# Kernel optimization log

Hardware: AMD Instinct MI355X
Metric: run time of the kernel (lower is better)

The kernel has to match this reference:

```python
import jax, jax.numpy as jnp
import numpy as np

NUM_EMBEDDINGS = 4096
EMBEDDING_DIM = 256
COMMITMENT_COST = 0.25
EPS = 1e-10


def setup_inputs() -> dict:
    key = jax.random.key(0)
    k1, k2 = jax.random.split(key)
    x = jax.random.normal(k1, (32, EMBEDDING_DIM, 32, 32), dtype=jnp.float32)
    # nn.Embedding weight init: uniform(-1/K, 1/K)
    lim = 1.0 / NUM_EMBEDDINGS
    weight = jax.random.uniform(k2, (NUM_EMBEDDINGS, EMBEDDING_DIM),
                                dtype=jnp.float32, minval=-lim, maxval=lim)
    return {"x": x, "weight": weight}


def reference(x, weight):
    B, D, H, W = x.shape
    K = weight.shape[0]
    # [B,D,H,W] -> [B,H,W,D] -> [N,D]
    flat = jnp.transpose(x, (0, 2, 3, 1)).reshape(-1, D)
    distances = (jnp.sum(flat * flat, axis=1, keepdims=True)
                 + jnp.sum(weight * weight, axis=1)
                 - 2.0 * jnp.matmul(flat, weight.T))  # [N,K]
    idx = jnp.argmin(distances, axis=1)  # [N]
    # direct gather == one_hot @ weight (same math, no NxK one-hot materialized)
    quantized = weight[idx].reshape(B, H, W, D)
    quantized = jnp.transpose(quantized, (0, 3, 1, 2))  # [B,D,H,W]
    quantized_st = x + jax.lax.stop_gradient(quantized - x)
    e_latent_loss = jnp.mean((jax.lax.stop_gradient(quantized) - x) ** 2)
    q_latent_loss = jnp.mean((quantized - jax.lax.stop_gradient(x)) ** 2)
    loss = q_latent_loss + COMMITMENT_COST * e_latent_loss
    # avg_probs = mean over tokens of one-hot encodings == normalized histogram
    counts = jnp.zeros((K,), dtype=flat.dtype).at[idx].add(1.0)
    avg_probs = counts / flat.shape[0]
    perplexity = jnp.exp(-jnp.sum(avg_probs * jnp.log(avg_probs + EPS)))
    encoding_indices = idx.reshape(B, H, W)
    return (quantized_st, loss, perplexity, encoding_indices)
```

## Files before the change

### kernel.cpp

```cpp
#include <hip/hip_runtime.h>
#include <math.h>
#include <stdint.h>

#define DIM 256
#define NUME 4096
#define NTOK 32768
#define NELEM 8388608
#define LOSS_OFF 8388608
#define PERP_OFF 8388609
#define IDX_OFF  8388610
#define MARGIN   4.0e-4f
#define ATHR_PAD 1.0e-4f
#define CAND_CAP 48
#define BOOT_TILES 32
#define TOKS 128

using short8 = __attribute__((ext_vector_type(8))) short;
using f32x16 = __attribute__((ext_vector_type(16))) float;

#define WAIT_VM4()   do { asm volatile("s_waitcnt vmcnt(4)" ::: "memory"); \
                          __builtin_amdgcn_sched_barrier(0); } while (0)
#define WAIT_VM0()   do { asm volatile("s_waitcnt vmcnt(0)" ::: "memory"); \
                          __builtin_amdgcn_sched_barrier(0); } while (0)
#define WAIT_LGKM0() do { asm volatile("s_waitcnt lgkmcnt(0)" ::: "memory"); \
                          __builtin_amdgcn_sched_barrier(0); } while (0)
#define BAR()        __builtin_amdgcn_s_barrier()

__device__ __forceinline__ uint16_t f2bf(float f) {
    uint32_t u = __float_as_uint(f);
    u += 0x7FFFu + ((u >> 16) & 1u);
    return (uint16_t)(u >> 16);
}
__device__ __forceinline__ void gload_lds16(const void* g, void* l) {
    __builtin_amdgcn_global_load_lds(
        (const __attribute__((address_space(1))) void*)g,
        (__attribute__((address_space(3))) void*)l, 16, 0, 0);
}

__global__ void vq_prep(const float* __restrict__ w, uint16_t* __restrict__ wb) {
    int gid = blockIdx.x * 256 + threadIdx.x;
    const float4* src = (const float4*)(w + (size_t)gid * 8);
    float4 a = src[0], c = src[1];
    uint4 o;
    o.x = (uint32_t)f2bf(a.x) | ((uint32_t)f2bf(a.y) << 16);
    o.y = (uint32_t)f2bf(a.z) | ((uint32_t)f2bf(a.w) << 16);
    o.z = (uint32_t)f2bf(c.x) | ((uint32_t)f2bf(c.y) << 16);
    o.w = (uint32_t)f2bf(c.z) | ((uint32_t)f2bf(c.w) << 16);
    *(uint4*)(wb + (size_t)gid * 8) = o;
}

__global__ __launch_bounds__(512, 1)
void vq_mfma(const float* __restrict__ x, const float* __restrict__ wt,
             const uint16_t* __restrict__ wb, float* __restrict__ out,
             int* __restrict__ counts, float* __restrict__ partials) {
    __shared__ __align__(16) char UB[65536];
    __shared__ float sxp[4][TOKS];
    __shared__ float sxS[TOKS];
    __shared__ unsigned gmU[TOKS];
    __shared__ unsigned candCnt[TOKS];
    __shared__ unsigned candL[TOKS * CAND_CAP];
    __shared__ int wIdxS[TOKS];
    __shared__ float lred[8];

    const int t    = threadIdx.x;
    const int lane = t & 63;
    const int wv   = t >> 6;
    const int wr   = wv >> 1, wc = wv & 1;
    const int l31  = lane & 31, hh = lane >> 5;
    const int wg   = blockIdx.x;
    const int n0   = wg << 7;
    const int b    = n0 >> 10;
    const int p0   = n0 & 1023;
    const float* xbase = x + (size_t)b * (DIM * 1024) + p0;

    if (t < TOKS) { gmU[t] = 0x7F7FFFFFu; candCnt[t] = 0; }

    {
        int tok = t & 127, w8 = t >> 7;
        const float* p = xbase + (size_t)(w8 * 64) * 1024 + tok;
        float s = 0.f;
        #pragma unroll
        for (int d = 0; d < 64; ++d) {
            float v = p[(size_t)d * 1024];
            s = fmaf(v, v, s);
            int byte = (tok << 9) + ((w8 * 64 + d) << 1);
            byte ^= ((tok & 15) << 4);
            *(uint16_t*)(UB + byte) = f2bf(v);
        }
        sxp[w8][tok] = s;
    }
    __syncthreads();
    if (t < TOKS) sxS[t] = (sxp[0][t] + sxp[1][t]) + (sxp[2][t] + sxp[3][t]);

    short8 aF[16];
    #pragma unroll
    for (int ks = 0; ks < 16; ++ks) {
        int row = wr * 32 + l31;
        int byte = (row << 9) + (ks << 5) + (hh << 4);
        byte ^= ((row & 15) << 4);
        aF[ks] = *(const short8*)(UB + byte);
    }
    __syncthreads();

    auto STAGE = [&](int k0, int half) {
        #pragma unroll
        for (int i = 0; i < 4; ++i) {
            int o16 = i * 512 + t;
            int code = o16 >> 5, u = o16 & 31;
            const char* src = (const char*)wb + ((size_t)(k0 + code) << 9)
                              + ((u ^ (code & 15)) << 4);
            gload_lds16(src, UB + (half << 15) + (o16 << 4));
        }
    };

    float run[16];
    #pragma unroll
    for (int rg = 0; rg < 16; ++rg) run[rg] = -3.0e38f;

    STAGE(0, 0);
    STAGE(64, 1);
    for (int tile = 0; tile < BOOT_TILES; ++tile) {
        if (tile < BOOT_TILES - 1) WAIT_VM4(); else WAIT_VM0();
        BAR();
        const int half = tile & 1;

        f32x16 acc = {0.f,0.f,0.f,0.f,0.f,0.f,0.f,0.f,
                      0.f,0.f,0.f,0.f,0.f,0.f,0.f,0.f};
        const int cr = wc * 32 + l31;
        const int bbase = (half << 15) + (cr << 9) + (hh << 4);
        const int bxor  = ((cr & 15) << 4);
        #pragma unroll
        for (int ks = 0; ks < 16; ++ks) {
            short8 bF = *(const short8*)(UB + ((bbase + (ks << 5)) ^ bxor));
            acc = __builtin_amdgcn_mfma_f32_32x32x16_bf16(aF[ks], bF, acc, 0, 0, 0);
        }
        #pragma unroll
        for (int rg = 0; rg < 16; ++rg) run[rg] = fmaxf(run[rg], acc[rg]);

        WAIT_LGKM0();
        BAR();
        if (tile + 2 < BOOT_TILES) STAGE((tile + 2) * 64, half);
    }

    #pragma unroll
    for (int rg = 0; rg < 16; ++rg) {
        float m = run[rg];
        #pragma unroll
        for (int sh = 1; sh < 32; sh <<= 1) m = fmaxf(m, __shfl_xor(m, sh, 64));
        if (l31 == 0) {
            int row = wr * 32 + (rg & 3) + 8 * (rg >> 2) + 4 * hh;
            float s = sxS[row] - 2.0f * m;
            atomicMin(&gmU[row], __float_as_uint(s));
        }
    }
    __syncthreads();

    float athr[16];
    #pragma unroll
    for (int rg = 0; rg < 16; ++rg) {
        int row = wr * 32 + (rg & 3) + 8 * (rg >> 2) + 4 * hh;
        athr[rg] = 0.5f * (sxS[row] - (__uint_as_float(gmU[row]) + MARGIN)) - ATHR_PAD;
    }

    STAGE(0, 0);
    STAGE(64, 1);
    for (int tile = 0; tile < 64; ++tile) {
        if (tile < 63) WAIT_VM4(); else WAIT_VM0();
        BAR();
        const int half = tile & 1;

        f32x16 acc = {0.f,0.f,0.f,0.f,0.f,0.f,0.f,0.f,
                      0.f,0.f,0.f,0.f,0.f,0.f,0.f,0.f};
        const int cr = wc * 32 + l31;
        const int bbase = (half << 15) + (cr << 9) + (hh << 4);
        const int bxor  = ((cr & 15) << 4);
        #pragma unroll
        for (int ks = 0; ks < 16; ++ks) {
            short8 bF = *(const short8*)(UB + ((bbase + (ks << 5)) ^ bxor));
            acc = __builtin_amdgcn_mfma_f32_32x32x16_bf16(aF[ks], bF, acc, 0, 0, 0);
        }
        #pragma unroll
        for (int rg = 0; rg < 16; ++rg) {
            if (acc[rg] >= athr[rg]) {
                int row = wr * 32 + (rg & 3) + 8 * (rg >> 2) + 4 * hh;
                int code = tile * 64 + wc * 32 + l31;
                unsigned s = atomicAdd(&candCnt[row], 1u);
                if (s < CAND_CAP) candL[row * CAND_CAP + s] = (unsigned)code;
            }
        }

        WAIT_LGKM0();
        BAR();
        if (tile + 2 < 64) STAGE((tile + 2) * 64, half);
    }

    float sqAcc = 0.f;
    for (int ch = 0; ch < 4; ++ch) {
        __syncthreads();
        {
            int dg = t >> 3, c = t & 7;
            #pragma unroll
            for (int it = 0; it < 4; ++it) {
                int d = it * 64 + dg;
                const float* row = xbase + (size_t)d * 1024 + ch * 32 + c * 4;
                float4 f0 = *(const float4*)(row);
                float vv[4] = {f0.x, f0.y, f0.z, f0.w};
                #pragma unroll
                for (int j = 0; j < 4; ++j) {
                    int tl = c * 4 + j;
                    *(float*)(UB + ((tl * 258 + d) << 2)) = vv[j];
                }
            }
        }
        __syncthreads();
        {
            const int grp = lane >> 4, gl = lane & 15;
            int tl = wv * 4 + grp;
            int tok = ch * 32 + tl;
            unsigned ncnt = candCnt[tok];
            int nc = (ncnt > CAND_CAP) ? 0 : (int)ncnt;
            float xr[16];
            const float* xs = (const float*)UB + tl * 258 + gl * 16;
            #pragma unroll
            for (int j = 0; j < 16; ++j) xr[j] = xs[j];
            float sxt = sxS[tok];
            float bs = 3.0e38f; int bi = 0;
            for (int ci = 0; ci < nc; ++ci) {
                int code = (int)candL[tok * CAND_CAP + ci];
                const float* wr_ = wt + (size_t)code * 256 + gl * 16;
                float p = 0.f;
                #pragma unroll
                for (int j = 0; j < 4; ++j) {
                    float4 w4 = *(const float4*)(wr_ + 4 * j);
                    p = fmaf(w4.x, xr[4 * j + 0], p);
                    p = fmaf(w4.y, xr[4 * j + 1], p);
                    p = fmaf(w4.z, xr[4 * j + 2], p);
                    p = fmaf(w4.w, xr[4 * j + 3], p);
                }
                #pragma unroll
                for (int sh = 1; sh < 16; sh <<= 1) p += __shfl_xor(p, sh, 64);
                float s = sxt - 2.0f * p;
                if (s < bs || (s == bs && code < bi)) { bs = s; bi = code; }
            }
            if (gl == 0 && nc > 0) wIdxS[tok] = bi;

            #pragma unroll
            for (int tt = 0; tt < 4; ++tt) {
                int tl2 = wv * 4 + tt;
                int tok2 = ch * 32 + tl2;
                if (candCnt[tok2] > CAND_CAP) {
                    float bs2 = 3.0e38f; int bi2 = 0;
                    for (int code = 0; code < NUME; ++code) {
                        float4 wv4 = *(const float4*)(wt + (size_t)code * 256 + lane * 4);
                        const float* xr2 = (const float*)UB + tl2 * 258 + lane * 4;
                        float p = wv4.x * xr2[0];
                        p = fmaf(wv4.y, xr2[1], p);
                        p = fmaf(wv4.z, xr2[2], p);
                        p = fmaf(wv4.w, xr2[3], p);
                        #pragma unroll
                        for (int sh = 1; sh < 64; sh <<= 1) p += __shfl_xor(p, sh, 64);
                        float s = sxS[tok2] - 2.0f * p;
                        if (s < bs2 || (s == bs2 && code < bi2)) { bs2 = s; bi2 = code; }
                    }
                    if (lane == 0) wIdxS[tok2] = bi2;
                }
            }
        }
        __syncthreads();
        {
            int tl = t & 31, db = (t >> 5) * 16;
            int idx = wIdxS[ch * 32 + tl];
            const float* wrow = wt + (size_t)idx * 256;
            float* op = out + (size_t)b * (DIM * 1024) + p0 + ch * 32 + tl;
            #pragma unroll
            for (int j = 0; j < 4; ++j) {
                int d = db + 4 * j;
                float4 q4 = *(const float4*)(wrow + d);
                const float* xr = (const float*)(UB + ((tl * 258 + d) << 2));
                float d0 = q4.x - xr[0], d1 = q4.y - xr[1];
                float d2 = q4.z - xr[2], d3 = q4.w - xr[3];
                sqAcc = fmaf(d0, d0, sqAcc); sqAcc = fmaf(d1, d1, sqAcc);
                sqAcc = fmaf(d2, d2, sqAcc); sqAcc = fmaf(d3, d3, sqAcc);
                op[(size_t)(d + 0) * 1024] = q4.x;
                op[(size_t)(d + 1) * 1024] = q4.y;
                op[(size_t)(d + 2) * 1024] = q4.z;
                op[(size_t)(d + 3) * 1024] = q4.w;
            }
        }
        if (t < 32) {
            int tok = ch * 32 + t;
            out[IDX_OFF + n0 + tok] = (float)wIdxS[tok];
            atomicAdd(&counts[wIdxS[tok]], 1);
        }
    }
    float sq = sqAcc;
    #pragma unroll
    for (int m = 32; m > 0; m >>= 1) sq += __shfl_down(sq, m, 64);
    if (lane == 0) lred[wv] = sq;
    __syncthreads();
    if (t == 0) {
        float s = ((lred[0] + lred[1]) + (lred[2] + lred[3]))
                + ((lred[4] + lred[5]) + (lred[6] + lred[7]));
        partials[wg] = s;
    }
}

#define TM 64
#define TN 64
#define DK 32
#define WS_PAD 68
__global__ __launch_bounds__(256, 2)
void vq_main_fb(const float* __restrict__ x, const float* __restrict__ wt,
                float* __restrict__ out, int* __restrict__ counts,
                float* __restrict__ partials) {
    __shared__ float As[DIM][TM];
    __shared__ float Ws[DK][WS_PAD];
    __shared__ float minv[TM];
    __shared__ int   mini[TM];
    __shared__ float sxp[4][TM];
    __shared__ float sxv[TM];
    __shared__ float lred[4];
    const int t = threadIdx.x, wg = blockIdx.x;
    const int n0 = wg * TM, b = n0 >> 10, p0 = n0 & 1023;
    const float* xb = x + (size_t)b * DIM * 1024 + p0;
    #pragma unroll
    for (int i = 0; i < 16; ++i) {
        int c = t + 256 * i, d = c >> 4, pg = (c & 15) << 2;
        *reinterpret_cast<float4*>(&As[d][pg]) =
            *reinterpret_cast<const float4*>(xb + (size_t)d * 1024 + pg);
    }
    if (t < TM) { minv[t] = 3.0e38f; mini[t] = 0; }
    __syncthreads();
    {
        int tok = t & 63, w = t >> 6;
        float p = 0.0f;
        #pragma unroll
        for (int d = 0; d < 64; ++d) { float v = As[w * 64 + d][tok]; p = fmaf(v, v, p); }
        sxp[w][tok] = p;
    }
    __syncthreads();
    if (t < TM) sxv[t] = (sxp[0][t] + sxp[1][t]) + (sxp[2][t] + sxp[3][t]);
    const int tx = t & 15, ty = t >> 4;
    for (int k0 = 0; k0 < NUME; k0 += TN) {
        float acc[4][4];
        #pragma unroll
        for (int i = 0; i < 4; ++i)
            #pragma unroll
            for (int j = 0; j < 4; ++j) acc[i][j] = 0.0f;
        for (int d0 = 0; d0 < DIM; d0 += DK) {
            __syncthreads();
            int r = t >> 3, dc = (t & 7) << 2;
            #pragma unroll
            for (int h = 0; h < 2; ++h) {
                float4 v = *reinterpret_cast<const float4*>(
                    wt + (size_t)(k0 + r + 32 * h) * DIM + d0 + dc);
                Ws[dc + 0][r + 32 * h] = v.x; Ws[dc + 1][r + 32 * h] = v.y;
                Ws[dc + 2][r + 32 * h] = v.z; Ws[dc + 3][r + 32 * h] = v.w;
            }
            __syncthreads();
            #pragma unroll
            for (int dd = 0; dd < DK; ++dd) {
                float4 a = *reinterpret_cast<const float4*>(&As[d0 + dd][ty << 2]);
                float4 w = *reinterpret_cast<const float4*>(&Ws[dd][tx << 2]);
                float av[4] = {a.x, a.y, a.z, a.w}, wv2[4] = {w.x, w.y, w.z, w.w};
                #pragma unroll
                for (int i = 0; i < 4; ++i)
                    #pragma unroll
                    for (int j = 0; j < 4; ++j) acc[i][j] = fmaf(av[i], wv2[j], acc[i][j]);
            }
        }
        #pragma unroll
        for (int i = 0; i < 4; ++i) {
            float sxt = sxv[(ty << 2) + i];
            float bv = 3.0e38f; int bi = 0;
            #pragma unroll
            for (int j = 0; j < 4; ++j) {
                float s = sxt - 2.0f * acc[i][j];
                int gi = k0 + (tx << 2) + j;
                if (s < bv) { bv = s; bi = gi; }
            }
            #pragma unroll
            for (int m = 1; m < 16; m <<= 1) {
                float ov = __shfl_xor(bv, m, 64); int oi = __shfl_xor(bi, m, 64);
                if (ov < bv || (ov == bv && oi < bi)) { bv = ov; bi = oi; }
            }
            if (tx == 0) {
                int pl = (ty << 2) + i;
                if (bv < minv[pl]) { minv[pl] = bv; mini[pl] = bi; }
            }
        }
    }
    __syncthreads();
    const int pg = (t & 15) << 2, db = t >> 4;
    int idx4[4];
    #pragma unroll
    for (int j = 0; j < 4; ++j) idx4[j] = mini[pg + j];
    float* outq = out + (size_t)b * DIM * 1024 + p0;
    float sq = 0.0f;
    #pragma unroll
    for (int i = 0; i < 16; ++i) {
        int d = db + (i << 4);
        float4 qv;
        qv.x = wt[(size_t)idx4[0] * DIM + d]; qv.y = wt[(size_t)idx4[1] * DIM + d];
        qv.z = wt[(size_t)idx4[2] * DIM + d]; qv.w = wt[(size_t)idx4[3] * DIM + d];
        float4 xa = *reinterpret_cast<const float4*>(&As[d][pg]);
        float d0_ = qv.x - xa.x, d1_ = qv.y - xa.y, d2_ = qv.z - xa.z, d3_ = qv.w - xa.w;
        sq = fmaf(d0_, d0_, sq); sq = fmaf(d1_, d1_, sq);
        sq = fmaf(d2_, d2_, sq); sq = fmaf(d3_, d3_, sq);
        *reinterpret_cast<float4*>(outq + (size_t)d * 1024 + pg) = qv;
    }
    const int lane = t & 63, wid = t >> 6;
    #pragma unroll
    for (int m = 32; m > 0; m >>= 1) sq += __shfl_down(sq, m, 64);
    if (lane == 0) lred[wid] = sq;
    __syncthreads();
    if (t == 0) partials[wg] = (lred[0] + lred[1]) + (lred[2] + lred[3]);
    if (t < TM) {
        atomicAdd(&counts[mini[t]], 1);
        out[IDX_OFF + n0 + t] = (float)mini[t];
    }
}

__global__ void vq_final(const int* __restrict__ counts,
                         const float* __restrict__ partials,
                         float* __restrict__ out, int npart) {
    __shared__ float red[256];
    int t = threadIdx.x;
    float s = 0.f;
    for (int i = t; i < npart; i += 256) s += partials[i];
    red[t] = s;
    __syncthreads();
    for (int m = 128; m > 0; m >>= 1) {
        if (t < m) red[t] += red[t + m];
        __syncthreads();
    }
    if (t == 0) out[LOSS_OFF] = 1.25f * red[0] / (float)NELEM;
    __syncthreads();
    float e = 0.0f;
    for (int c = t; c < NUME; c += 256) {
        float p = (float)counts[c] * (1.0f / (float)NTOK);
        e += p * logf(p + 1e-10f);
    }
    red[t] = e;
    __syncthreads();
    for (int m = 128; m > 0; m >>= 1) {
        if (t < m) red[t] += red[t + m];
        __syncthreads();
    }
    if (t == 0) out[PERP_OFF] = expf(-red[0]);
}

extern "C" void kernel_launch(void* const* d_in, const int* in_sizes, int n_in,
                              void* d_out, int out_size, void* d_ws, size_t ws_size,
                              hipStream_t stream) {
    const float* x  = (const float*)d_in[0];
    const float* wt = (const float*)d_in[1];
    float* out = (float*)d_out;
    const size_t WB_BYTES = (size_t)NUME * DIM * 2;
    const size_t NEED = WB_BYTES + 16384 + 2048;

    if (ws_size >= NEED) {
        uint16_t* wb  = (uint16_t*)d_ws;
        int* counts   = (int*)((char*)d_ws + WB_BYTES);
        float* partials = (float*)((char*)d_ws + WB_BYTES + 16384);
        hipMemsetAsync((char*)d_ws + WB_BYTES, 0, 16384 + 2048, stream);
        vq_prep<<<512, 256, 0, stream>>>(wt, wb);
        vq_mfma<<<NTOK / TOKS, 512, 0, stream>>>(x, wt, wb, out, counts, partials);
        vq_final<<<1, 256, 0, stream>>>(counts, partials, out, NTOK / TOKS);
    } else {
        int* counts   = (int*)d_ws;
        float* partials = (float*)((char*)d_ws + 16384);
        hipMemsetAsync(d_ws, 0, 16384 + 2048, stream);
        vq_main_fb<<<NTOK / TM, 256, 0, stream>>>(x, wt, out, counts, partials);
        vq_final<<<1, 256, 0, stream>>>(counts, partials, out, NTOK / TM);
    }
}
```

Baseline: 194.4 us.

## Halve workgroup to 4 waves, each computing two 32-row MFMA tiles per B fragment

The MFMA kernel now runs with 256 threads instead of 512, and each wave holds two A-fragment sets (64 token rows), so every B fragment read from LDS feeds two MFMAs. Staging, x-loading, rerank and output loops are widened so 4 waves cover the same work. The intent is to halve LDS B-fragment traffic per MFMA and improve MFMA issue density. In exchange it roughly doubles register pressure (accumulators, A fragments, thresholds) and halves the waves available to hide latency in the scalar rerank and epilogue phases.

```diff
diff --git a/kernel.cpp b/kernel.cpp
--- a/kernel.cpp
+++ b/kernel.cpp
@@ -18,7 +18,7 @@
 using short8 = __attribute__((ext_vector_type(8))) short;
 using f32x16 = __attribute__((ext_vector_type(16))) float;
 
-#define WAIT_VM4()   do { asm volatile("s_waitcnt vmcnt(4)" ::: "memory"); \
+#define WAIT_VM8()   do { asm volatile("s_waitcnt vmcnt(8)" ::: "memory"); \
                           __builtin_amdgcn_sched_barrier(0); } while (0)
 #define WAIT_VM0()   do { asm volatile("s_waitcnt vmcnt(0)" ::: "memory"); \
                           __builtin_amdgcn_sched_barrier(0); } while (0)
@@ -49,18 +49,18 @@
     *(uint4*)(wb + (size_t)gid * 8) = o;
 }
 
-__global__ __launch_bounds__(512, 1)
+__global__ __launch_bounds__(256, 1)
 void vq_mfma(const float* __restrict__ x, const float* __restrict__ wt,
              const uint16_t* __restrict__ wb, float* __restrict__ out,
              int* __restrict__ counts, float* __restrict__ partials) {
     __shared__ __align__(16) char UB[65536];
-    __shared__ float sxp[4][TOKS];
+    __shared__ float sxp[2][TOKS];
     __shared__ float sxS[TOKS];
     __shared__ unsigned gmU[TOKS];
     __shared__ unsigned candCnt[TOKS];
     __shared__ unsigned candL[TOKS * CAND_CAP];
     __shared__ int wIdxS[TOKS];
-    __shared__ float lred[8];
+    __shared__ float lred[4];
 
     const int t    = threadIdx.x;
     const int lane = t & 63;
@@ -77,35 +77,37 @@
 
     {
         int tok = t & 127, w8 = t >> 7;
-        const float* p = xbase + (size_t)(w8 * 64) * 1024 + tok;
+        const float* p = xbase + (size_t)(w8 * 128) * 1024 + tok;
         float s = 0.f;
         #pragma unroll
-        for (int d = 0; d < 64; ++d) {
+        for (int d = 0; d < 128; ++d) {
             float v = p[(size_t)d * 1024];
             s = fmaf(v, v, s);
-            int byte = (tok << 9) + ((w8 * 64 + d) << 1);
+            int byte = (tok << 9) + ((w8 * 128 + d) << 1);
             byte ^= ((tok & 15) << 4);
             *(uint16_t*)(UB + byte) = f2bf(v);
         }
         sxp[w8][tok] = s;
     }
     __syncthreads();
-    if (t < TOKS) sxS[t] = (sxp[0][t] + sxp[1][t]) + (sxp[2][t] + sxp[3][t]);
-
-    short8 aF[16];
-    #pragma unroll
-    for (int ks = 0; ks < 16; ++ks) {
-        int row = wr * 32 + l31;
-        int byte = (row << 9) + (ks << 5) + (hh << 4);
-        byte ^= ((row & 15) << 4);
-        aF[ks] = *(const short8*)(UB + byte);
-    }
+    if (t < TOKS) sxS[t] = sxp[0][t] + sxp[1][t];
+
+    short8 aF[2][16];
+    #pragma unroll
+    for (int rf = 0; rf < 2; ++rf)
+        #pragma unroll
+        for (int ks = 0; ks < 16; ++ks) {
+            int row = wr * 64 + rf * 32 + l31;
+            int byte = (row << 9) + (ks << 5) + (hh << 4);
+            byte ^= ((row & 15) << 4);
+            aF[rf][ks] = *(const short8*)(UB + byte);
+        }
     __syncthreads();
 
     auto STAGE = [&](int k0, int half) {
         #pragma unroll
-        for (int i = 0; i < 4; ++i) {
-            int o16 = i * 512 + t;
+        for (int i = 0; i < 8; ++i) {
+            int o16 = i * 256 + t;
             int code = o16 >> 5, u = o16 & 31;
             const char* src = (const char*)wb + ((size_t)(k0 + code) << 9)
                               + ((u ^ (code & 15)) << 4);
@@ -113,29 +115,37 @@
         }
     };
 
-    float run[16];
-    #pragma unroll
-    for (int rg = 0; rg < 16; ++rg) run[rg] = -3.0e38f;
+    float run[2][16];
+    #pragma unroll
+    for (int rf = 0; rf < 2; ++rf)
+        #pragma unroll
+        for (int rg = 0; rg < 16; ++rg) run[rf][rg] = -3.0e38f;
 
     STAGE(0, 0);
     STAGE(64, 1);
     for (int tile = 0; tile < BOOT_TILES; ++tile) {
-        if (tile < BOOT_TILES - 1) WAIT_VM4(); else WAIT_VM0();
+        if (tile < BOOT_TILES - 1) WAIT_VM8(); else WAIT_VM0();
         BAR();
         const int half = tile & 1;
 
-        f32x16 acc = {0.f,0.f,0.f,0.f,0.f,0.f,0.f,0.f,
-                      0.f,0.f,0.f,0.f,0.f,0.f,0.f,0.f};
+        f32x16 acc0 = {0.f,0.f,0.f,0.f,0.f,0.f,0.f,0.f,
+                       0.f,0.f,0.f,0.f,0.f,0.f,0.f,0.f};
+        f32x16 acc1 = {0.f,0.f,0.f,0.f,0.f,0.f,0.f,0.f,
+                       0.f,0.f,0.f,0.f,0.f,0.f,0.f,0.f};
         const int cr = wc * 32 + l31;
         const int bbase = (half << 15) + (cr << 9) + (hh << 4);
         const int bxor  = ((cr & 15) << 4);
         #pragma unroll
         for (int ks = 0; ks < 16; ++ks) {
             short8 bF = *(const short8*)(UB + ((bbase + (ks << 5)) ^ bxor));
-            acc = __builtin_amdgcn_mfma_f32_32x32x16_bf16(aF[ks], bF, acc, 0, 0, 0);
-        }
-        #pragma unroll
-        for (int rg = 0; rg < 16; ++rg) run[rg] = fmaxf(run[rg], acc[rg]);
+            acc0 = __builtin_amdgcn_mfma_f32_32x32x16_bf16(aF[0][ks], bF, acc0, 0, 0, 0);
+            acc1 = __builtin_amdgcn_mfma_f32_32x32x16_bf16(aF[1][ks], bF, acc1, 0, 0, 0);
+        }
+        #pragma unroll
+        for (int rg = 0; rg < 16; ++rg) {
+            run[0][rg] = fmaxf(run[0][rg], acc0[rg]);
+            run[1][rg] = fmaxf(run[1][rg], acc1[rg]);
+        }
 
         WAIT_LGKM0();
         BAR();
@@ -143,46 +153,59 @@
     }
 
     #pragma unroll
-    for (int rg = 0; rg < 16; ++rg) {
-        float m = run[rg];
-        #pragma unroll
-        for (int sh = 1; sh < 32; sh <<= 1) m = fmaxf(m, __shfl_xor(m, sh, 64));
-        if (l31 == 0) {
-            int row = wr * 32 + (rg & 3) + 8 * (rg >> 2) + 4 * hh;
-            float s = sxS[row] - 2.0f * m;
-            atomicMin(&gmU[row], __float_as_uint(s));
-        }
-    }
-    __syncthreads();
-
-    float athr[16];
-    #pragma unroll
-    for (int rg = 0; rg < 16; ++rg) {
-        int row = wr * 32 + (rg & 3) + 8 * (rg >> 2) + 4 * hh;
-        athr[rg] = 0.5f * (sxS[row] - (__uint_as_float(gmU[row]) + MARGIN)) - ATHR_PAD;
-    }
+    for (int rf = 0; rf < 2; ++rf)
+        #pragma unroll
+        for (int rg = 0; rg < 16; ++rg) {
+            float m = run[rf][rg];
+            #pragma unroll
+            for (int sh = 1; sh < 32; sh <<= 1) m = fmaxf(m, __shfl_xor(m, sh, 64));
+            if (l31 == 0) {
+                int row = wr * 64 + rf * 32 + (rg & 3) + 8 * (rg >> 2) + 4 * hh;
+                float s = sxS[row] - 2.0f * m;
+                atomicMin(&gmU[row], __float_as_uint(s));
+            }
+        }
+    __syncthreads();
+
+    float athr[2][16];
+    #pragma unroll
+    for (int rf = 0; rf < 2; ++rf)
+        #pragma unroll
+        for (int rg = 0; rg < 16; ++rg) {
+            int row = wr * 64 + rf * 32 + (rg & 3) + 8 * (rg >> 2) + 4 * hh;
+            athr[rf][rg] = 0.5f * (sxS[row] - (__uint_as_float(gmU[row]) + MARGIN)) - ATHR_PAD;
+        }
 
     STAGE(0, 0);
     STAGE(64, 1);
     for (int tile = 0; tile < 64; ++tile) {
-        if (tile < 63) WAIT_VM4(); else WAIT_VM0();
+        if (tile < 63) WAIT_VM8(); else WAIT_VM0();
         BAR();
         const int half = tile & 1;
 
-        f32x16 acc = {0.f,0.f,0.f,0.f,0.f,0.f,0.f,0.f,
-                      0.f,0.f,0.f,0.f,0.f,0.f,0.f,0.f};
+        f32x16 acc0 = {0.f,0.f,0.f,0.f,0.f,0.f,0.f,0.f,
+                       0.f,0.f,0.f,0.f,0.f,0.f,0.f,0.f};
+        f32x16 acc1 = {0.f,0.f,0.f,0.f,0.f,0.f,0.f,0.f,
+                       0.f,0.f,0.f,0.f,0.f,0.f,0.f,0.f};
         const int cr = wc * 32 + l31;
         const int bbase = (half << 15) + (cr << 9) + (hh << 4);
         const int bxor  = ((cr & 15) << 4);
         #pragma unroll
         for (int ks = 0; ks < 16; ++ks) {
             short8 bF = *(const short8*)(UB + ((bbase + (ks << 5)) ^ bxor));
-            acc = __builtin_amdgcn_mfma_f32_32x32x16_bf16(aF[ks], bF, acc, 0, 0, 0);
+            acc0 = __builtin_amdgcn_mfma_f32_32x32x16_bf16(aF[0][ks], bF, acc0, 0, 0, 0);
+            acc1 = __builtin_amdgcn_mfma_f32_32x32x16_bf16(aF[1][ks], bF, acc1, 0, 0, 0);
         }
         #pragma unroll
         for (int rg = 0; rg < 16; ++rg) {
-            if (acc[rg] >= athr[rg]) {
-                int row = wr * 32 + (rg & 3) + 8 * (rg >> 2) + 4 * hh;
+            if (acc0[rg] >= athr[0][rg]) {
+                int row = wr * 64 + (rg & 3) + 8 * (rg >> 2) + 4 * hh;
+                int code = tile * 64 + wc * 32 + l31;
+                unsigned s = atomicAdd(&candCnt[row], 1u);
+                if (s < CAND_CAP) candL[row * CAND_CAP + s] = (unsigned)code;
+            }
+            if (acc1[rg] >= athr[1][rg]) {
+                int row = wr * 64 + 32 + (rg & 3) + 8 * (rg >> 2) + 4 * hh;
                 int code = tile * 64 + wc * 32 + l31;
                 unsigned s = atomicAdd(&candCnt[row], 1u);
                 if (s < CAND_CAP) candL[row * CAND_CAP + s] = (unsigned)code;
@@ -198,16 +221,17 @@
     for (int ch = 0; ch < 4; ++ch) {
         __syncthreads();
         {
-            int dg = t >> 3, c = t & 7;
+            int dg = t >> 2, c = t & 3;
             #pragma unroll
             for (int it = 0; it < 4; ++it) {
                 int d = it * 64 + dg;
-                const float* row = xbase + (size_t)d * 1024 + ch * 32 + c * 4;
+                const float* row = xbase + (size_t)d * 1024 + ch * 32 + c * 8;
                 float4 f0 = *(const float4*)(row);
-                float vv[4] = {f0.x, f0.y, f0.z, f0.w};
+                float4 f1 = *(const float4*)(row + 4);
+                float vv[8] = {f0.x, f0.y, f0.z, f0.w, f1.x, f1.y, f1.z, f1.w};
                 #pragma unroll
-                for (int j = 0; j < 4; ++j) {
-                    int tl = c * 4 + j;
+                for (int j = 0; j < 8; ++j) {
+                    int tl = c * 8 + j;
                     *(float*)(UB + ((tl * 258 + d) << 2)) = vv[j];
                 }
             }
@@ -215,38 +239,39 @@
         __syncthreads();
         {
             const int grp = lane >> 4, gl = lane & 15;
-            int tl = wv * 4 + grp;
-            int tok = ch * 32 + tl;
-            unsigned ncnt = candCnt[tok];
-            int nc = (ncnt > CAND_CAP) ? 0 : (int)ncnt;
-            float xr[16];
-            const float* xs = (const float*)UB + tl * 258 + gl * 16;
-            #pragma unroll
-            for (int j = 0; j < 16; ++j) xr[j] = xs[j];
-            float sxt = sxS[tok];
-            float bs = 3.0e38f; int bi = 0;
-            for (int ci = 0; ci < nc; ++ci) {
-                int code = (int)candL[tok * CAND_CAP + ci];
-                const float* wr_ = wt + (size_t)code * 256 + gl * 16;
-                float p = 0.f;
+            #pragma unroll
+            for (int ti = 0; ti < 2; ++ti) {
+                int tl = wv * 4 + grp + ti * 16;
+                int tok = ch * 32 + tl;
+                unsigned ncnt = candCnt[tok];
+                int nc = (ncnt > CAND_CAP) ? 0 : (int)ncnt;
+                float xr[16];
+                const float* xs = (const float*)UB + tl * 258 + gl * 16;
                 #pragma unroll
-                for (int j = 0; j < 4; ++j) {
-                    float4 w4 = *(const float4*)(wr_ + 4 * j);
-                    p = fmaf(w4.x, xr[4 * j + 0], p);
-                    p = fmaf(w4.y, xr[4 * j + 1], p);
-                    p = fmaf(w4.z, xr[4 * j + 2], p);
-                    p = fmaf(w4.w, xr[4 * j + 3], p);
+                for (int j = 0; j < 16; ++j) xr[j] = xs[j];
+                float sxt = sxS[tok];
+                float bs = 3.0e38f; int bi = 0;
+                for (int ci = 0; ci < nc; ++ci) {
+                    int code = (int)candL[tok * CAND_CAP + ci];
+                    const float* wr_ = wt + (size_t)code * 256 + gl * 16;
+                    float p = 0.f;
+                    #pragma unroll
+                    for (int j = 0; j < 4; ++j) {
+                        float4 w4 = *(const float4*)(wr_ + 4 * j);
+                        p = fmaf(w4.x, xr[4 * j + 0], p);
+                        p = fmaf(w4.y, xr[4 * j + 1], p);
+                        p = fmaf(w4.z, xr[4 * j + 2], p);
+                        p = fmaf(w4.w, xr[4 * j + 3], p);
+                    }
+                    #pragma unroll
+                    for (int sh = 1; sh < 16; sh <<= 1) p += __shfl_xor(p, sh, 64);
+                    float s = sxt - 2.0f * p;
+                    if (s < bs || (s == bs && code < bi)) { bs = s; bi = code; }
                 }
-                #pragma unroll
-                for (int sh = 1; sh < 16; sh <<= 1) p += __shfl_xor(p, sh, 64);
-                float s = sxt - 2.0f * p;
-                if (s < bs || (s == bs && code < bi)) { bs = s; bi = code; }
-            }
-            if (gl == 0 && nc > 0) wIdxS[tok] = bi;
-
-            #pragma unroll
-            for (int tt = 0; tt < 4; ++tt) {
-                int tl2 = wv * 4 + tt;
+                if (gl == 0 && nc > 0) wIdxS[tok] = bi;
+            }
+            for (int tt = 0; tt < 8; ++tt) {
+                int tl2 = wv * 4 + (tt & 3) + (tt >> 2) * 16;
                 int tok2 = ch * 32 + tl2;
                 if (candCnt[tok2] > CAND_CAP) {
                     float bs2 = 3.0e38f; int bi2 = 0;
@@ -268,12 +293,12 @@
         }
         __syncthreads();
         {
-            int tl = t & 31, db = (t >> 5) * 16;
+            int tl = t & 31, db = (t >> 5) * 32;
             int idx = wIdxS[ch * 32 + tl];
             const float* wrow = wt + (size_t)idx * 256;
             float* op = out + (size_t)b * (DIM * 1024) + p0 + ch * 32 + tl;
             #pragma unroll
-            for (int j = 0; j < 4; ++j) {
+            for (int j = 0; j < 8; ++j) {
                 int d = db + 4 * j;
                 float4 q4 = *(const float4*)(wrow + d);
                 const float* xr = (const float*)(UB + ((tl * 258 + d) << 2));
@@ -298,11 +323,7 @@
     for (int m = 32; m > 0; m >>= 1) sq += __shfl_down(sq, m, 64);
     if (lane == 0) lred[wv] = sq;
     __syncthreads();
-    if (t == 0) {
-        float s = ((lred[0] + lred[1]) + (lred[2] + lred[3]))
-                + ((lred[4] + lred[5]) + (lred[6] + lred[7]));
-        partials[wg] = s;
-    }
+    if (t == 0) partials[wg] = (lred[0] + lred[1]) + (lred[2] + lred[3]);
 }
 
 #define TM 64
@@ -465,7 +486,7 @@
         float* partials = (float*)((char*)d_ws + WB_BYTES + 16384);
         hipMemsetAsync((char*)d_ws + WB_BYTES, 0, 16384 + 2048, stream);
         vq_prep<<<512, 256, 0, stream>>>(wt, wb);
-        vq_mfma<<<NTOK / TOKS, 512, 0, stream>>>(x, wt, wb, out, counts, partials);
+        vq_mfma<<<NTOK / TOKS, 256, 0, stream>>>(x, wt, wb, out, counts, partials);
         vq_final<<<1, 256, 0, stream>>>(counts, partials, out, NTOK / TOKS);
     } else {
         int* counts   = (int*)d_ws;
```

Measured after the change: 269.9 us. +38.9%, slower.
